# Performance work log

Hardware: AMD Instinct MI355X
Metric: run time of the kernel (lower is better)

## Reference

```python
import jax, jax.numpy as jnp
import numpy as np
from functools import partial

N_ITER = 200  # LML(n_iter=200)


def sq_dists(Xi, x):
    # Xi: [N, n], x: [B, n] -> squared euclidean dists [B, N] (torch.cdist ** 2)
    x2 = jnp.sum(x * x, axis=1, keepdims=True)          # [B, 1]
    m2 = jnp.sum(Xi * Xi, axis=1)                        # [N]
    d = x2 + m2[None, :] - 2.0 * (x @ Xi.T)
    return jnp.maximum(d, 0.0)


def _lml_solve(x, k):
    # LML projection: y = sigmoid(x + nu), nu s.t. sum(y) = k; bisection on nu.
    x_sorted = -jnp.sort(-x, axis=1)                     # descending
    lo = -x_sorted[:, k - 1] - 7.0
    hi = -x_sorted[:, k] + 7.0

    def body(i, bounds):
        lo, hi = bounds
        mid = 0.5 * (lo + hi)
        f = jnp.sum(jax.nn.sigmoid(x + mid[:, None]), axis=1) - k
        lo = jnp.where(f < 0, mid, lo)
        hi = jnp.where(f < 0, hi, mid)
        return lo, hi

    lo, hi = jax.lax.fori_loop(0, N_ITER, body, (lo, hi))
    nu = 0.5 * (lo + hi)
    return jax.nn.sigmoid(x + nu[:, None])


@partial(jax.custom_vjp, nondiff_argnums=(1,))
def lml(x, k):
    return _lml_solve(x, k)


def _lml_fwd(x, k):
    y = _lml_solve(x, k)
    return y, y


def _lml_bwd(k, y, g):
    # implicit grad: dy = s*(dx - dnu), dnu = sum(s*dx)/sum(s), s = y(1-y)
    s = y * (1.0 - y)
    dnu = jnp.sum(s * g, axis=1, keepdims=True) / jnp.sum(s, axis=1, keepdims=True)
    return (s * (g - dnu),)


lml.defvjp(_lml_fwd, _lml_bwd)


def k_softmax(beta, x, k):
    # x: [B, N] (= -dists) -> [B, N, k]
    cols = [jax.nn.softmax(beta * x, axis=1)]
    last = cols[0]
    for i in range(1, k):
        new = lml(beta * x, i + 1)
        cols.append(new - last)
        last = new
    return jnp.stack(cols, axis=2)


def hopfield(Xi, x, beta):
    return jax.nn.softmax(-beta * sq_dists(Xi, x), axis=1) @ Xi


def k_hopfield_batch(Xi, x, k, beta, hopfield_steps):
    dists = sq_dists(Xi, x)                              # [B, N]
    ksm = k_softmax(beta, -dists, k)                     # [B, N, k]
    result = jnp.einsum('nd,bnk->bdk', Xi, ksm)          # Xi.T @ ksm -> [B, n, k]
    for _ in range(hopfield_steps):
        result = jnp.stack(
            [hopfield(Xi, result[:, :, j], beta) for j in range(k)], axis=2)
    return result


def setup_inputs() -> dict:
    key = jax.random.key(0)
    kx, km = jax.random.split(key)
    return {
        'x': jax.random.normal(kx, (2048, 512), dtype=jnp.float32),
        'memories': jax.random.normal(km, (8192, 512), dtype=jnp.float32),
        'k': 5,
        'beta': 1,
        'hopfield_steps': 2,
    }


def reference(x, memories, k, beta, hopfield_steps):
    return k_hopfield_batch(memories, x, k, beta, hopfield_steps)
```

## Files before the change

### kernel.cpp

```cpp
#include <hip/hip_runtime.h>
#include <hip/hip_bf16.h>


constexpr int   Bq    = 2048;
constexpr int   Nm    = 8192;
constexpr int   Dd    = 512;
constexpr int   KK    = 5;
constexpr float BETA  = 1.0f;
constexpr int   STEPS = 2;
constexpr int   KS    = 8;
constexpr size_t PL   = (size_t)Bq * Dd;

#define DEV static __device__ __forceinline__

DEV float b2f(ushort u) { unsigned v = ((unsigned)u) << 16; float f; __builtin_memcpy(&f, &v, 4); return f; }
DEV ushort f2b(float f) { __hip_bfloat16 h = __float2bfloat16(f); ushort u; __builtin_memcpy(&u, &h, 2); return u; }
DEV float ldin(const void* p, int isf, size_t idx) {
    return isf ? ((const float*)p)[idx] : b2f(((const ushort*)p)[idx]);
}

__global__ __launch_bounds__(256) void detect_k(const ushort* __restrict__ xin,
                                                int* __restrict__ flag) {
    __shared__ int sb;
    if (threadIdx.x == 0) sb = 0;
    __syncthreads();
    int bad = 0;
    for (int i = threadIdx.x; i < 1024; i += 256) {
        float v = b2f(xin[i]);
        if (!(fabsf(v) < 64.0f)) bad = 1;
    }
    if (bad) atomicOr(&sb, 1);
    __syncthreads();
    if (threadIdx.x == 0) flag[0] = sb;
}

__global__ __launch_bounds__(256) void norms_k(const void* __restrict__ xin,
                                               const void* __restrict__ memin,
                                               const int* __restrict__ flag,
                                               float* __restrict__ x2,
                                               float* __restrict__ m2) {
    int row = blockIdx.x;
    int isf = flag[0];
    const void* src; size_t base; float* dst;
    if (row < Nm) { src = memin; base = (size_t)row * Dd; dst = m2 + row; }
    else          { src = xin; base = (size_t)(row - Nm) * Dd; dst = x2 + (row - Nm); }
    int tid = threadIdx.x, lane = tid & 63, wave = tid >> 6;
    float s = 0.f;
    for (int i = tid; i < Dd; i += 256) { float v = ldin(src, isf, base + i); s += v * v; }
    for (int off = 32; off; off >>= 1) s += __shfl_down(s, off, 64);
    __shared__ float ws[4];
    if (lane == 0) ws[wave] = s;
    __syncthreads();
    if (tid == 0) dst[0] = ws[0] + ws[1] + ws[2] + ws[3];
}

__global__ __launch_bounds__(256) void distF2_k(const void* __restrict__ A,
                                                const int* __restrict__ flag, int aForceF,
                                                const void* __restrict__ memin,
                                                float* __restrict__ S,
                                                const float* __restrict__ a2,
                                                const float* __restrict__ m2,
                                                int ab0, float negBeta) {
    __shared__ float As[16][68];
    __shared__ float Bs[16][68];
    const int tid = threadIdx.x, tx = tid & 15, ty = tid >> 4;
    const int m0 = blockIdx.y * 64, n0 = blockIdx.x * 64;
    const int isfA = aForceF ? 1 : flag[0];
    const int isfB = flag[0];

    float acc[4][4];
#pragma unroll
    for (int i = 0; i < 4; ++i)
#pragma unroll
        for (int j = 0; j < 4; ++j) acc[i][j] = 0.f;

    for (int d0 = 0; d0 < Dd; d0 += 16) {
#pragma unroll
        for (int c = tid; c < 1024; c += 256) {
            int r = c >> 4, k = c & 15;
            As[k][r] = ldin(A, isfA, (size_t)(ab0 + m0 + r) * Dd + d0 + k);
            Bs[k][r] = ldin(memin, isfB, (size_t)(n0 + r) * Dd + d0 + k);
        }
        __syncthreads();
#pragma unroll
        for (int k = 0; k < 16; ++k) {
            float4 av = *(const float4*)&As[k][ty * 4];
            float4 bv = *(const float4*)&Bs[k][tx * 4];
            float a[4] = {av.x, av.y, av.z, av.w};
            float b[4] = {bv.x, bv.y, bv.z, bv.w};
#pragma unroll
            for (int i = 0; i < 4; ++i)
#pragma unroll
                for (int j = 0; j < 4; ++j) acc[i][j] = fmaf(a[i], b[j], acc[i][j]);
        }
        __syncthreads();
    }
#pragma unroll
    for (int i = 0; i < 4; ++i) {
        int m = m0 + ty * 4 + i;
        float4 o;
        float* po = (float*)&o;
#pragma unroll
        for (int j = 0; j < 4; ++j) {
            float d = a2[m] + m2[n0 + tx * 4 + j] - 2.0f * acc[i][j];
            po[j] = negBeta * fmaxf(d, 0.0f);
        }
        *(float4*)&S[(size_t)m * Nm + n0 + tx * 4] = o;
    }
}

template <int TRF>
__global__ __launch_bounds__(256) void wgemmG_k(const float* __restrict__ Sx,
                                                const void* __restrict__ memin,
                                                const int* __restrict__ flag,
                                                const float* __restrict__ rowpar,
                                                float* __restrict__ part, int planeSz) {
    __shared__ float Ws[16][68];
    __shared__ float Bs[16][68];
    const int tid = threadIdx.x, tx = tid & 15, ty = tid >> 4;
    const int d0 = blockIdx.x * 64, b0 = blockIdx.y * 64;
    const int kz = blockIdx.z * (Nm / KS);
    const int isf = flag[0];

    float acc[4][4];
#pragma unroll
    for (int i = 0; i < 4; ++i)
#pragma unroll
        for (int j = 0; j < 4; ++j) acc[i][j] = 0.f;

    for (int nc = kz; nc < kz + Nm / KS; nc += 16) {
#pragma unroll
        for (int c = tid; c < 1024; c += 256) {
            int r = c >> 4, k = c & 15;
            float s = Sx[(size_t)(b0 + r) * Nm + nc + k];
            float p0 = rowpar[(b0 + r) * 2 + 0];
            float w;
            if constexpr (TRF == 1) w = expf(s - p0) * rowpar[(b0 + r) * 2 + 1];
            else                    w = 1.0f / (1.0f + expf(-(s + p0)));
            Ws[k][r] = w;
            int kk = c >> 6, dd = c & 63;
            Bs[kk][dd] = ldin(memin, isf, (size_t)(nc + kk) * Dd + d0 + dd);
        }
        __syncthreads();
#pragma unroll
        for (int k = 0; k < 16; ++k) {
            float4 av = *(const float4*)&Ws[k][ty * 4];
            float4 bv = *(const float4*)&Bs[k][tx * 4];
            float a[4] = {av.x, av.y, av.z, av.w};
            float b[4] = {bv.x, bv.y, bv.z, bv.w};
#pragma unroll
            for (int i = 0; i < 4; ++i)
#pragma unroll
                for (int j = 0; j < 4; ++j) acc[i][j] = fmaf(a[i], b[j], acc[i][j]);
        }
        __syncthreads();
    }
    float* pz = part + (size_t)blockIdx.z * planeSz;
#pragma unroll
    for (int i = 0; i < 4; ++i) {
        float4 o = {acc[i][0], acc[i][1], acc[i][2], acc[i][3]};
        *(float4*)&pz[(size_t)(b0 + ty * 4 + i) * Dd + d0 + tx * 4] = o;
    }
}

__global__ __launch_bounds__(256) void reduceN_k(const float* __restrict__ part,
                                                 float* __restrict__ Rj,
                                                 float* __restrict__ r2w, int doNorm,
                                                 int planeSz) {
    int row = blockIdx.x, tid = threadIdx.x, lane = tid & 63, wave = tid >> 6;
    float sq = 0.f;
    for (int e = tid; e < Dd; e += 256) {
        float s = 0.f;
#pragma unroll
        for (int z = 0; z < KS; ++z) s += part[(size_t)z * planeSz + (size_t)row * Dd + e];
        Rj[(size_t)row * Dd + e] = s;
        sq += s * s;
    }
    if (doNorm) {
        for (int off = 32; off; off >>= 1) sq += __shfl_down(sq, off, 64);
        __shared__ float ws[4];
        if (lane == 0) ws[wave] = sq;
        __syncthreads();
        if (tid == 0) r2w[row] = ws[0] + ws[1] + ws[2] + ws[3];
    }
}

__global__ __launch_bounds__(256) void rowstats_k(const float* __restrict__ S,
                                                  float* __restrict__ stats) {
    int b = blockIdx.x, tid = threadIdx.x, lane = tid & 63, wave = tid >> 6;
    __shared__ float cbuf[1024];
    __shared__ int   ccnt;
    __shared__ float tops[256 * 6];
    __shared__ float stop[6];
    __shared__ float wred[16];
    __shared__ float bcast[5];
    const float* srow = S + (size_t)b * Nm;

    float tt[6];
#pragma unroll
    for (int q = 0; q < 6; ++q) tt[q] = -3.4e38f;
    for (int i = tid; i < Nm; i += 256) {
        float v = srow[i];
        if (v > tt[5]) {
            tt[5] = v;
#pragma unroll
            for (int q = 5; q > 0; --q)
                if (tt[q] > tt[q - 1]) { float tm = tt[q]; tt[q] = tt[q - 1]; tt[q - 1] = tm; }
        }
    }
#pragma unroll
    for (int q = 0; q < 6; ++q) tops[tid * 6 + q] = tt[q];
    if (tid == 0) ccnt = 0;
    __syncthreads();
    if (tid == 0) {
        float mt[6];
#pragma unroll
        for (int q = 0; q < 6; ++q) mt[q] = -3.4e38f;
        for (int i = 0; i < 256 * 6; ++i) {
            float v = tops[i];
            if (v > mt[5]) {
                mt[5] = v;
#pragma unroll
                for (int q = 5; q > 0; --q)
                    if (mt[q] > mt[q - 1]) { float tm = mt[q]; mt[q] = mt[q - 1]; mt[q - 1] = tm; }
            }
        }
#pragma unroll
        for (int q = 0; q < 6; ++q) stop[q] = mt[q];
    }
    __syncthreads();

    float smax = stop[0];
    float cutoff = stop[5] - 40.0f;
    float p = 0.f;
    for (int i = tid; i < Nm; i += 256) {
        float v = srow[i];
        p += expf(v - smax);
        if (v >= cutoff) {
            int idx = atomicAdd(&ccnt, 1);
            if (idx < 1024) cbuf[idx] = v;
        }
    }
    for (int off = 32; off; off >>= 1) p += __shfl_down(p, off, 64);
    if (lane == 0) wred[wave] = p;
    __syncthreads();
    if (tid == 0) bcast[4] = wred[0] + wred[1] + wred[2] + wred[3];
    __syncthreads();
    float denom = bcast[4];
    int cnt = min(ccnt, 1024);

    float lo[4], hi[4];
#pragma unroll
    for (int q = 0; q < 4; ++q) { lo[q] = -stop[q + 1] - 7.0f; hi[q] = -stop[q + 2] + 7.0f; }
    for (int it = 0; it < 48; ++it) {
        float mid[4], pp[4] = {0.f, 0.f, 0.f, 0.f};
#pragma unroll
        for (int q = 0; q < 4; ++q) mid[q] = 0.5f * (lo[q] + hi[q]);
        for (int i = tid; i < cnt; i += 256) {
            float v = cbuf[i];
#pragma unroll
            for (int q = 0; q < 4; ++q) pp[q] += 1.0f / (1.0f + expf(-(v + mid[q])));
        }
#pragma unroll
        for (int q = 0; q < 4; ++q) {
            float s = pp[q];
            for (int off = 32; off; off >>= 1) s += __shfl_down(s, off, 64);
            if (lane == 0) wred[wave * 4 + q] = s;
        }
        __syncthreads();
        if (tid == 0)
#pragma unroll
            for (int q = 0; q < 4; ++q) bcast[q] = wred[q] + wred[4 + q] + wred[8 + q] + wred[12 + q];
        __syncthreads();
#pragma unroll
        for (int q = 0; q < 4; ++q) {
            float f = bcast[q] - (float)(q + 2);
            if (f < 0.f) lo[q] = mid[q]; else hi[q] = mid[q];
        }
        __syncthreads();
    }
    if (tid == 0) {
        stats[b * 6 + 0] = smax;
        stats[b * 6 + 1] = denom;
#pragma unroll
        for (int q = 0; q < 4; ++q) stats[b * 6 + 2 + q] = 0.5f * (lo[q] + hi[q]);
    }
}

__global__ __launch_bounds__(256) void rowpar_stage1_k(const float* __restrict__ stats,
                                                       float* __restrict__ rowpar, int jj) {
    int b = blockIdx.x * 256 + threadIdx.x;
    if (b >= Bq) return;
    if (jj == 0) {
        rowpar[b * 2 + 0] = stats[b * 6 + 0];
        rowpar[b * 2 + 1] = 1.0f / stats[b * 6 + 1];
    } else {
        rowpar[b * 2 + 0] = stats[b * 6 + 1 + jj];
        rowpar[b * 2 + 1] = 0.0f;
    }
}

__global__ __launch_bounds__(256) void rowmax_denom_k(const float* __restrict__ S,
                                                      float* __restrict__ rowpar) {
    int b = blockIdx.x, tid = threadIdx.x, lane = tid & 63, wave = tid >> 6;
    __shared__ float wred[4];
    __shared__ float bc[1];
    const float* srow = S + (size_t)b * Nm;
    float mx = -3.4e38f;
    for (int i = tid; i < Nm; i += 256) mx = fmaxf(mx, srow[i]);
    for (int off = 32; off; off >>= 1) mx = fmaxf(mx, __shfl_down(mx, off, 64));
    if (lane == 0) wred[wave] = mx;
    __syncthreads();
    if (tid == 0) bc[0] = fmaxf(fmaxf(wred[0], wred[1]), fmaxf(wred[2], wred[3]));
    __syncthreads();
    mx = bc[0];
    float p = 0.f;
    for (int i = tid; i < Nm; i += 256) p += expf(srow[i] - mx);
    for (int off = 32; off; off >>= 1) p += __shfl_down(p, off, 64);
    __syncthreads();
    if (lane == 0) wred[wave] = p;
    __syncthreads();
    if (tid == 0) {
        rowpar[b * 2 + 0] = mx;
        rowpar[b * 2 + 1] = 1.0f / (wred[0] + wred[1] + wred[2] + wred[3]);
    }
}

__global__ __launch_bounds__(256) void combine_k(float* __restrict__ R,
                                                 float* __restrict__ r2all) {
    int row = blockIdx.x, tid = threadIdx.x, lane = tid & 63, wave = tid >> 6;
    float sq[5] = {0.f, 0.f, 0.f, 0.f, 0.f};
    for (int e = tid; e < Dd; e += 256) {
        size_t idx = (size_t)row * Dd + e;
        float r0 = R[idx], r1 = R[PL + idx], r2v = R[2 * PL + idx],
              r3 = R[3 * PL + idx], r4 = R[4 * PL + idx];
        float o1 = r1 - r0, o2 = r2v - r1, o3 = r3 - r2v, o4 = r4 - r3;
        R[PL + idx] = o1; R[2 * PL + idx] = o2; R[3 * PL + idx] = o3; R[4 * PL + idx] = o4;
        sq[0] += r0 * r0; sq[1] += o1 * o1; sq[2] += o2 * o2; sq[3] += o3 * o3; sq[4] += o4 * o4;
    }
    __shared__ float ws[5][4];
#pragma unroll
    for (int j = 0; j < 5; ++j) {
        float s = sq[j];
        for (int off = 32; off; off >>= 1) s += __shfl_down(s, off, 64);
        if (lane == 0) ws[j][wave] = s;
    }
    __syncthreads();
    if (tid < 5) r2all[tid * Bq + row] = ws[tid][0] + ws[tid][1] + ws[tid][2] + ws[tid][3];
}

__global__ __launch_bounds__(256) void final_k(const float* __restrict__ R,
                                               void* __restrict__ out,
                                               const int* __restrict__ flag) {
    size_t idx = (size_t)blockIdx.x * 256 + threadIdx.x;
    bool isf = flag[0] != 0;
#pragma unroll
    for (int j = 0; j < KK; ++j) {
        float v = R[(size_t)j * PL + idx];
        if (isf) ((float*)out)[idx * KK + j] = v;
        else     ((ushort*)out)[idx * KK + j] = f2b(v);
    }
}

extern "C" void kernel_launch(void* const* d_in, const int* in_sizes, int n_in,
                              void* d_out, int out_size, void* d_ws, size_t ws_size,
                              hipStream_t stream) {
    const void* xin   = d_in[0];
    const void* memin = d_in[1];

    const size_t MiB = 1048576ull, KiB = 1024ull;
    char* ws = (char*)d_ws;
    float* R     = (float*)(ws + 0);
    float* m2    = (float*)(ws + 20 * MiB);
    float* x2    = (float*)(ws + 20 * MiB + 32 * KiB);
    float* stats = (float*)(ws + 20 * MiB + 48 * KiB);
    float* rpar  = (float*)(ws + 20 * MiB + 96 * KiB);
    int*   flag  = (int*)  (ws + 20 * MiB + 112 * KiB);
    float* r2all = (float*)(ws + 20 * MiB + 128 * KiB);
    float* S     = (float*)(ws + 20 * MiB + 256 * KiB);

    float* part = (float*)d_out;

    int Bc = 128;
    const int cand[4] = {1024, 512, 256, 128};
    for (int i = 0; i < 4; ++i)
        if (20 * MiB + 256 * KiB + (size_t)cand[i] * Nm * 4 <= ws_size) { Bc = cand[i]; break; }
    const int nChunk = Bq / Bc;
    const int planeSz = Bc * Dd;

    detect_k<<<1, 256, 0, stream>>>((const ushort*)xin, flag);
    norms_k<<<Nm + Bq, 256, 0, stream>>>(xin, memin, flag, x2, m2);

    for (int c = 0; c < nChunk; ++c) {
        int b0 = c * Bc;
        distF2_k<<<dim3(Nm / 64, Bc / 64), 256, 0, stream>>>(
            xin, flag, 0, memin, S, x2 + b0, m2, b0, -BETA);
        rowstats_k<<<Bc, 256, 0, stream>>>(S, stats + (size_t)b0 * 6);
        for (int jj = 0; jj < KK; ++jj) {
            float* Rj = R + (size_t)jj * PL + (size_t)b0 * Dd;
            rowpar_stage1_k<<<Bq / 256, 256, 0, stream>>>(stats, rpar, jj);
            if (jj == 0)
                wgemmG_k<1><<<dim3(Dd / 64, Bc / 64, KS), 256, 0, stream>>>(
                    S, memin, flag, rpar + (size_t)b0 * 2, part, planeSz);
            else
                wgemmG_k<2><<<dim3(Dd / 64, Bc / 64, KS), 256, 0, stream>>>(
                    S, memin, flag, rpar + (size_t)b0 * 2, part, planeSz);
            reduceN_k<<<Bc, 256, 0, stream>>>(part, Rj, nullptr, 0, planeSz);
        }
    }
    combine_k<<<Bq, 256, 0, stream>>>(R, r2all);

    for (int st = 0; st < STEPS; ++st) {
        for (int jj = 0; jj < KK; ++jj) {
            float* Rj = R + (size_t)jj * PL;
            float* r2j = r2all + (size_t)jj * Bq;
            for (int c = 0; c < nChunk; ++c) {
                int b0 = c * Bc;
                distF2_k<<<dim3(Nm / 64, Bc / 64), 256, 0, stream>>>(
                    Rj, flag, 1, memin, S, r2j + b0, m2, b0, -BETA);
                rowmax_denom_k<<<Bc, 256, 0, stream>>>(S, rpar + (size_t)b0 * 2);
                wgemmG_k<1><<<dim3(Dd / 64, Bc / 64, KS), 256, 0, stream>>>(
                    S, memin, flag, rpar + (size_t)b0 * 2, part, planeSz);
                reduceN_k<<<Bc, 256, 0, stream>>>(
                    part, Rj + (size_t)b0 * Dd, r2j + b0, 1, planeSz);
            }
        }
    }
    final_k<<<(int)(PL / 256), 256, 0, stream>>>(R, d_out, flag);
}
```

Before: 10.11 ms.

## Use split-bf16 MFMA GEMMs with precomputed hi/lo operand planes

Adds a new path that splits fp32 operands into bf16 high and low parts and runs the distance and weighted-sum GEMMs on MFMA bf16 instructions, using three products to approximate fp32 accuracy. The memory matrix is converted and transposed once up front, and the softmax/sigmoid weights are materialised as hi/lo bf16 planes before each GEMM. This replaces the scalar fp32 tiled GEMMs with matrix-core work. In exchange it adds conversion passes, extra workspace, and a small loss of precision from dropping the lo*lo term.

```diff
diff --git a/kernel.cpp b/kernel.cpp
--- a/kernel.cpp
+++ b/kernel.cpp
@@ -12,6 +12,10 @@
 constexpr size_t PL   = (size_t)Bq * Dd;
 
 #define DEV static __device__ __forceinline__
+
+typedef __attribute__((ext_vector_type(8))) short           short8v;
+typedef __attribute__((ext_vector_type(8))) unsigned short  u16x8;
+typedef __attribute__((ext_vector_type(4))) float           f32x4;
 
 DEV float b2f(ushort u) { unsigned v = ((unsigned)u) << 16; float f; __builtin_memcpy(&f, &v, 4); return f; }
 DEV ushort f2b(float f) { __hip_bfloat16 h = __float2bfloat16(f); ushort u; __builtin_memcpy(&u, &h, 2); return u; }
@@ -54,6 +58,480 @@
     if (tid == 0) dst[0] = ws[0] + ws[1] + ws[2] + ws[3];
 }
 
+
+__global__ __launch_bounds__(256) void convHL_k(const void* __restrict__ src,
+                                                const int* __restrict__ flag,
+                                                ushort* __restrict__ H,
+                                                ushort* __restrict__ L,
+                                                int nQuads, int qoff) {
+    int isf = flag[0];
+    for (int i = blockIdx.x * 256 + threadIdx.x; i < nQuads; i += gridDim.x * 256) {
+        float v[4];
+        if (isf) {
+            float4 t = ((const float4*)src)[qoff + i];
+            v[0] = t.x; v[1] = t.y; v[2] = t.z; v[3] = t.w;
+        } else {
+            ushort4 t = ((const ushort4*)src)[qoff + i];
+            v[0] = b2f(t.x); v[1] = b2f(t.y); v[2] = b2f(t.z); v[3] = b2f(t.w);
+        }
+        ushort4 h, l;
+        ushort* hp = (ushort*)&h; ushort* lp = (ushort*)&l;
+#pragma unroll
+        for (int j = 0; j < 4; ++j) {
+            ushort hu = f2b(v[j]);
+            hp[j] = hu;
+            lp[j] = f2b(v[j] - b2f(hu));
+        }
+        ((ushort4*)H)[i] = h;
+        ((ushort4*)L)[i] = l;
+    }
+}
+
+__global__ __launch_bounds__(256) void convT_k(const void* __restrict__ memin,
+                                               const int* __restrict__ flag,
+                                               ushort* __restrict__ TH,
+                                               ushort* __restrict__ TL) {
+    __shared__ float tile[64][65];
+    const int isf = flag[0];
+    const int n0 = blockIdx.x * 64, d0 = blockIdx.y * 64;
+    const int tid = threadIdx.x;
+    {
+        const int r = tid >> 2, cseg = tid & 3;
+#pragma unroll
+        for (int j = 0; j < 16; ++j)
+            tile[r][cseg * 16 + j] = ldin(memin, isf, (size_t)(n0 + r) * Dd + d0 + cseg * 16 + j);
+    }
+    __syncthreads();
+    {
+        const int drow = tid >> 2, nseg = tid & 3;
+        u16x8 h[2], l[2];
+#pragma unroll
+        for (int c = 0; c < 2; ++c)
+#pragma unroll
+            for (int j = 0; j < 8; ++j) {
+                float v = tile[nseg * 16 + c * 8 + j][drow];
+                ushort hu = f2b(v);
+                h[c][j] = hu;
+                l[c][j] = f2b(v - b2f(hu));
+            }
+        size_t base = (size_t)(d0 + drow) * Nm + n0 + nseg * 16;
+#pragma unroll
+        for (int c = 0; c < 2; ++c) {
+            *(u16x8*)&TH[base + c * 8] = h[c];
+            *(u16x8*)&TL[base + c * 8] = l[c];
+        }
+    }
+}
+
+__global__ __launch_bounds__(256) void distMF2_k(const ushort* __restrict__ Ah,
+                                                 const ushort* __restrict__ Al,
+                                                 const ushort* __restrict__ Mh,
+                                                 const ushort* __restrict__ Ml,
+                                                 float* __restrict__ S,
+                                                 const float* __restrict__ a2,
+                                                 const float* __restrict__ m2,
+                                                 int ab0, float negBeta) {
+    __shared__ ushort TA[2][4][128][8];
+    __shared__ ushort TB[2][4][128][8];
+    const int tid = threadIdx.x, lane = tid & 63, wid = tid >> 6;
+    const int wm = wid >> 1, wn = wid & 1;
+    const int m0 = blockIdx.y * 128, n0 = blockIdx.x * 128;
+    const int srow = tid & 127, kb = tid >> 7;
+    const size_t baseA = (size_t)(ab0 + m0 + srow) * Dd;
+    const size_t baseB = (size_t)(n0 + srow) * Dd;
+
+    f32x4 acc[4][4];
+    const f32x4 z = {0.f, 0.f, 0.f, 0.f};
+#pragma unroll
+    for (int i = 0; i < 4; ++i)
+#pragma unroll
+        for (int j = 0; j < 4; ++j) acc[i][j] = z;
+
+    for (int k0 = 0; k0 < Dd; k0 += 32) {
+        u16x8 rah0 = *(const u16x8*)&Ah[baseA + k0 + kb * 8];
+        u16x8 rah1 = *(const u16x8*)&Ah[baseA + k0 + (kb + 2) * 8];
+        u16x8 ral0 = *(const u16x8*)&Al[baseA + k0 + kb * 8];
+        u16x8 ral1 = *(const u16x8*)&Al[baseA + k0 + (kb + 2) * 8];
+        u16x8 rbh0 = *(const u16x8*)&Mh[baseB + k0 + kb * 8];
+        u16x8 rbh1 = *(const u16x8*)&Mh[baseB + k0 + (kb + 2) * 8];
+        u16x8 rbl0 = *(const u16x8*)&Ml[baseB + k0 + kb * 8];
+        u16x8 rbl1 = *(const u16x8*)&Ml[baseB + k0 + (kb + 2) * 8];
+        __syncthreads();
+        *(u16x8*)&TA[0][kb][srow][0]     = rah0;
+        *(u16x8*)&TA[0][kb + 2][srow][0] = rah1;
+        *(u16x8*)&TA[1][kb][srow][0]     = ral0;
+        *(u16x8*)&TA[1][kb + 2][srow][0] = ral1;
+        *(u16x8*)&TB[0][kb][srow][0]     = rbh0;
+        *(u16x8*)&TB[0][kb + 2][srow][0] = rbh1;
+        *(u16x8*)&TB[1][kb][srow][0]     = rbl0;
+        *(u16x8*)&TB[1][kb + 2][srow][0] = rbl1;
+        __syncthreads();
+
+        const int rl = lane & 15, kc = lane >> 4;
+        short8v ah[4], al[4];
+#pragma unroll
+        for (int fm = 0; fm < 4; ++fm) {
+            const int ra_ = wm * 64 + fm * 16 + rl;
+            ah[fm] = *(const short8v*)&TA[0][kc][ra_][0];
+            al[fm] = *(const short8v*)&TA[1][kc][ra_][0];
+        }
+#pragma unroll
+        for (int fn = 0; fn < 4; ++fn) {
+            const int rb_ = wn * 64 + fn * 16 + rl;
+            short8v bh = *(const short8v*)&TB[0][kc][rb_][0];
+            short8v bl = *(const short8v*)&TB[1][kc][rb_][0];
+#pragma unroll
+            for (int fm = 0; fm < 4; ++fm) {
+                acc[fm][fn] = __builtin_amdgcn_mfma_f32_16x16x32_bf16(ah[fm], bh, acc[fm][fn], 0, 0, 0);
+                acc[fm][fn] = __builtin_amdgcn_mfma_f32_16x16x32_bf16(al[fm], bh, acc[fm][fn], 0, 0, 0);
+                acc[fm][fn] = __builtin_amdgcn_mfma_f32_16x16x32_bf16(ah[fm], bl, acc[fm][fn], 0, 0, 0);
+            }
+        }
+    }
+
+    const int col = lane & 15, r0 = (lane >> 4) * 4;
+#pragma unroll
+    for (int fm = 0; fm < 4; ++fm)
+#pragma unroll
+        for (int fn = 0; fn < 4; ++fn) {
+            const int n = n0 + wn * 64 + fn * 16 + col;
+            const float mm2 = m2[n];
+#pragma unroll
+            for (int q = 0; q < 4; ++q) {
+                const int m = m0 + wm * 64 + fm * 16 + r0 + q;
+                const float d = a2[m] + mm2 - 2.0f * acc[fm][fn][q];
+                S[(size_t)m * Nm + n] = negBeta * fmaxf(d, 0.0f);
+            }
+        }
+}
+
+__global__ __launch_bounds__(256) void wconv_k(const float* __restrict__ S,
+                                               const float* __restrict__ par6,
+                                               const float* __restrict__ par2,
+                                               ushort* __restrict__ Wh,
+                                               ushort* __restrict__ Wl,
+                                               int mode, int jj) {
+    const int b = blockIdx.x, tid = threadIdx.x;
+    float p0 = 0.f, p1 = 0.f;
+    if (mode == 0)      { p0 = par6[b * 6 + 0]; p1 = 1.0f / par6[b * 6 + 1]; }
+    else if (mode == 1) { p0 = par6[b * 6 + 1 + jj]; }
+    else                { p0 = par2[b * 2 + 0]; p1 = par2[b * 2 + 1]; }
+    const float4* sp = (const float4*)(S + (size_t)b * Nm);
+    ushort* whp = Wh + (size_t)b * Nm;
+    ushort* wlp = Wl + (size_t)b * Nm;
+#pragma unroll
+    for (int r = 0; r < 8; ++r) {
+        const int qi = r * 256 + tid;
+        float4 t = sp[qi];
+        float s4[4] = {t.x, t.y, t.z, t.w};
+        ushort4 oh, ol;
+        ushort* ohp = (ushort*)&oh;
+        ushort* olp = (ushort*)&ol;
+#pragma unroll
+        for (int j = 0; j < 4; ++j) {
+            float w;
+            if (mode == 1) w = 1.0f / (1.0f + expf(-(s4[j] + p0)));
+            else           w = expf(s4[j] - p0) * p1;
+            ushort hu = f2b(w);
+            ohp[j] = hu;
+            olp[j] = f2b(w - b2f(hu));
+        }
+        ((ushort4*)whp)[qi] = oh;
+        ((ushort4*)wlp)[qi] = ol;
+    }
+}
+
+__global__ __launch_bounds__(256) void wgemm3_k(const ushort* __restrict__ Wh,
+                                                const ushort* __restrict__ Wl,
+                                                const ushort* __restrict__ MTh,
+                                                const ushort* __restrict__ MTl,
+                                                float* __restrict__ part,
+                                                int planeSz, int nzLen) {
+    __shared__ ushort TW[2][4][128][8];
+    __shared__ ushort TB[2][4][64][8];
+    const int tid = threadIdx.x, lane = tid & 63, wid = tid >> 6;
+    const int wm = wid >> 1, wn = wid & 1;
+    const int d0 = blockIdx.x * 64, b0 = blockIdx.y * 128;
+    const int nz0 = blockIdx.z * nzLen;
+
+    const int wrow = tid & 127, wkb = tid >> 7;
+    const int brow = tid & 63,  bkc = tid >> 6;
+    const size_t baseW = (size_t)(b0 + wrow) * Nm;
+    const size_t baseB = (size_t)(d0 + brow) * Nm;
+
+    f32x4 acc[4][2];
+    const f32x4 z = {0.f, 0.f, 0.f, 0.f};
+#pragma unroll
+    for (int i = 0; i < 4; ++i)
+#pragma unroll
+        for (int j = 0; j < 2; ++j) acc[i][j] = z;
+
+    for (int nc = nz0; nc < nz0 + nzLen; nc += 32) {
+        u16x8 rwh0 = *(const u16x8*)&Wh[baseW + nc + wkb * 8];
+        u16x8 rwh1 = *(const u16x8*)&Wh[baseW + nc + (wkb + 2) * 8];
+        u16x8 rwl0 = *(const u16x8*)&Wl[baseW + nc + wkb * 8];
+        u16x8 rwl1 = *(const u16x8*)&Wl[baseW + nc + (wkb + 2) * 8];
+        u16x8 rbh  = *(const u16x8*)&MTh[baseB + nc + bkc * 8];
+        u16x8 rbl  = *(const u16x8*)&MTl[baseB + nc + bkc * 8];
+        __syncthreads();
+        *(u16x8*)&TW[0][wkb][wrow][0]     = rwh0;
+        *(u16x8*)&TW[0][wkb + 2][wrow][0] = rwh1;
+        *(u16x8*)&TW[1][wkb][wrow][0]     = rwl0;
+        *(u16x8*)&TW[1][wkb + 2][wrow][0] = rwl1;
+        *(u16x8*)&TB[0][bkc][brow][0]     = rbh;
+        *(u16x8*)&TB[1][bkc][brow][0]     = rbl;
+        __syncthreads();
+
+        const int rl = lane & 15, kc = lane >> 4;
+        short8v wfh[4], wfl[4];
+#pragma unroll
+        for (int fm = 0; fm < 4; ++fm) {
+            const int rw_ = wm * 64 + fm * 16 + rl;
+            wfh[fm] = *(const short8v*)&TW[0][kc][rw_][0];
+            wfl[fm] = *(const short8v*)&TW[1][kc][rw_][0];
+        }
+#pragma unroll
+        for (int fn = 0; fn < 2; ++fn) {
+            const int rd_ = wn * 32 + fn * 16 + rl;
+            short8v bh = *(const short8v*)&TB[0][kc][rd_][0];
+            short8v bl = *(const short8v*)&TB[1][kc][rd_][0];
+#pragma unroll
+            for (int fm = 0; fm < 4; ++fm) {
+                acc[fm][fn] = __builtin_amdgcn_mfma_f32_16x16x32_bf16(wfh[fm], bh, acc[fm][fn], 0, 0, 0);
+                acc[fm][fn] = __builtin_amdgcn_mfma_f32_16x16x32_bf16(wfl[fm], bh, acc[fm][fn], 0, 0, 0);
+                acc[fm][fn] = __builtin_amdgcn_mfma_f32_16x16x32_bf16(wfh[fm], bl, acc[fm][fn], 0, 0, 0);
+            }
+        }
+    }
+
+    float* pz = part + (size_t)blockIdx.z * planeSz;
+    const int col = lane & 15, r0 = (lane >> 4) * 4;
+#pragma unroll
+    for (int fm = 0; fm < 4; ++fm)
+#pragma unroll
+        for (int fn = 0; fn < 2; ++fn) {
+            const int dc = d0 + wn * 32 + fn * 16 + col;
+#pragma unroll
+            for (int q = 0; q < 4; ++q) {
+                const int br = b0 + wm * 64 + fm * 16 + r0 + q;
+                pz[(size_t)br * Dd + dc] = acc[fm][fn][q];
+            }
+        }
+}
+
+__global__ __launch_bounds__(256) void reduceHL_k(const float* __restrict__ part,
+                                                  ushort* __restrict__ Rh,
+                                                  ushort* __restrict__ Rl,
+                                                  float* __restrict__ r2w, int doNorm,
+                                                  int planeSz, int ks) {
+    int row = blockIdx.x, tid = threadIdx.x, lane = tid & 63, wave = tid >> 6;
+    float sq = 0.f;
+    for (int e = tid; e < Dd; e += 256) {
+        float s = 0.f;
+        for (int z = 0; z < ks; ++z) s += part[(size_t)z * planeSz + (size_t)row * Dd + e];
+        ushort h = f2b(s);
+        Rh[(size_t)row * Dd + e] = h;
+        Rl[(size_t)row * Dd + e] = f2b(s - b2f(h));
+        sq += s * s;
+    }
+    if (doNorm) {
+        for (int off = 32; off; off >>= 1) sq += __shfl_down(sq, off, 64);
+        __shared__ float ws[4];
+        if (lane == 0) ws[wave] = sq;
+        __syncthreads();
+        if (tid == 0) r2w[row] = ws[0] + ws[1] + ws[2] + ws[3];
+    }
+}
+
+__global__ __launch_bounds__(256) void combineHL_k(ushort* __restrict__ rhl,
+                                                   float* __restrict__ r2all) {
+    int row = blockIdx.x, tid = threadIdx.x, lane = tid & 63, wave = tid >> 6;
+    float sq[5] = {0.f, 0.f, 0.f, 0.f, 0.f};
+    for (int e = tid; e < Dd; e += 256) {
+        size_t idx = (size_t)row * Dd + e;
+        float v[5];
+#pragma unroll
+        for (int j = 0; j < 5; ++j)
+            v[j] = b2f(rhl[(size_t)j * 2 * PL + idx]) + b2f(rhl[(size_t)j * 2 * PL + PL + idx]);
+        float o[5];
+        o[0] = v[0];
+        o[1] = v[1] - v[0]; o[2] = v[2] - v[1]; o[3] = v[3] - v[2]; o[4] = v[4] - v[3];
+#pragma unroll
+        for (int j = 1; j < 5; ++j) {
+            ushort h = f2b(o[j]);
+            rhl[(size_t)j * 2 * PL + idx] = h;
+            rhl[(size_t)j * 2 * PL + PL + idx] = f2b(o[j] - b2f(h));
+        }
+#pragma unroll
+        for (int j = 0; j < 5; ++j) sq[j] += o[j] * o[j];
+    }
+    __shared__ float ws[5][4];
+#pragma unroll
+    for (int j = 0; j < 5; ++j) {
+        float s = sq[j];
+        for (int off = 32; off; off >>= 1) s += __shfl_down(s, off, 64);
+        if (lane == 0) ws[j][wave] = s;
+    }
+    __syncthreads();
+    if (tid < 5) r2all[tid * Bq + row] = ws[tid][0] + ws[tid][1] + ws[tid][2] + ws[tid][3];
+}
+
+__global__ __launch_bounds__(256) void finalHL_k(const ushort* __restrict__ rhl,
+                                                 void* __restrict__ out,
+                                                 const int* __restrict__ flag) {
+    size_t idx = (size_t)blockIdx.x * 256 + threadIdx.x;
+    bool isf = flag[0] != 0;
+#pragma unroll
+    for (int j = 0; j < KK; ++j) {
+        float v = b2f(rhl[(size_t)j * 2 * PL + idx]) + b2f(rhl[(size_t)j * 2 * PL + PL + idx]);
+        if (isf) ((float*)out)[idx * KK + j] = v;
+        else     ((ushort*)out)[idx * KK + j] = f2b(v);
+    }
+}
+
+
+__global__ __launch_bounds__(256) void rowstats_k(const float* __restrict__ S,
+                                                  float* __restrict__ stats) {
+    int b = blockIdx.x, tid = threadIdx.x, lane = tid & 63, wave = tid >> 6;
+    __shared__ float cbuf[1024];
+    __shared__ int   ccnt;
+    __shared__ float tops[256 * 6];
+    __shared__ float stop[6];
+    __shared__ float wred[16];
+    __shared__ float bcast[5];
+    const float* srow = S + (size_t)b * Nm;
+
+    float tt[6];
+#pragma unroll
+    for (int q = 0; q < 6; ++q) tt[q] = -3.4e38f;
+    for (int i = tid; i < Nm; i += 256) {
+        float v = srow[i];
+        if (v > tt[5]) {
+            tt[5] = v;
+#pragma unroll
+            for (int q = 5; q > 0; --q)
+                if (tt[q] > tt[q - 1]) { float tm = tt[q]; tt[q] = tt[q - 1]; tt[q - 1] = tm; }
+        }
+    }
+#pragma unroll
+    for (int q = 0; q < 6; ++q) tops[tid * 6 + q] = tt[q];
+    if (tid == 0) ccnt = 0;
+    __syncthreads();
+    if (tid == 0) {
+        float mt[6];
+#pragma unroll
+        for (int q = 0; q < 6; ++q) mt[q] = -3.4e38f;
+        for (int i = 0; i < 256 * 6; ++i) {
+            float v = tops[i];
+            if (v > mt[5]) {
+                mt[5] = v;
+#pragma unroll
+                for (int q = 5; q > 0; --q)
+                    if (mt[q] > mt[q - 1]) { float tm = mt[q]; mt[q] = mt[q - 1]; mt[q - 1] = tm; }
+            }
+        }
+#pragma unroll
+        for (int q = 0; q < 6; ++q) stop[q] = mt[q];
+    }
+    __syncthreads();
+
+    float smax = stop[0];
+    float cutoff = stop[5] - 40.0f;
+    float p = 0.f;
+    for (int i = tid; i < Nm; i += 256) {
+        float v = srow[i];
+        p += expf(v - smax);
+        if (v >= cutoff) {
+            int idx = atomicAdd(&ccnt, 1);
+            if (idx < 1024) cbuf[idx] = v;
+        }
+    }
+    for (int off = 32; off; off >>= 1) p += __shfl_down(p, off, 64);
+    if (lane == 0) wred[wave] = p;
+    __syncthreads();
+    if (tid == 0) bcast[4] = wred[0] + wred[1] + wred[2] + wred[3];
+    __syncthreads();
+    float denom = bcast[4];
+    int cnt = min(ccnt, 1024);
+
+    float lo[4], hi[4];
+#pragma unroll
+    for (int q = 0; q < 4; ++q) { lo[q] = -stop[q + 1] - 7.0f; hi[q] = -stop[q + 2] + 7.0f; }
+    for (int it = 0; it < 48; ++it) {
+        float mid[4], pp[4] = {0.f, 0.f, 0.f, 0.f};
+#pragma unroll
+        for (int q = 0; q < 4; ++q) mid[q] = 0.5f * (lo[q] + hi[q]);
+        for (int i = tid; i < cnt; i += 256) {
+            float v = cbuf[i];
+#pragma unroll
+            for (int q = 0; q < 4; ++q) pp[q] += 1.0f / (1.0f + expf(-(v + mid[q])));
+        }
+#pragma unroll
+        for (int q = 0; q < 4; ++q) {
+            float s = pp[q];
+            for (int off = 32; off; off >>= 1) s += __shfl_down(s, off, 64);
+            if (lane == 0) wred[wave * 4 + q] = s;
+        }
+        __syncthreads();
+        if (tid == 0)
+#pragma unroll
+            for (int q = 0; q < 4; ++q) bcast[q] = wred[q] + wred[4 + q] + wred[8 + q] + wred[12 + q];
+        __syncthreads();
+#pragma unroll
+        for (int q = 0; q < 4; ++q) {
+            float f = bcast[q] - (float)(q + 2);
+            if (f < 0.f) lo[q] = mid[q]; else hi[q] = mid[q];
+        }
+        __syncthreads();
+    }
+    if (tid == 0) {
+        stats[b * 6 + 0] = smax;
+        stats[b * 6 + 1] = denom;
+#pragma unroll
+        for (int q = 0; q < 4; ++q) stats[b * 6 + 2 + q] = 0.5f * (lo[q] + hi[q]);
+    }
+}
+
+__global__ __launch_bounds__(256) void rowpar_stage1_k(const float* __restrict__ stats,
+                                                       float* __restrict__ rowpar, int jj) {
+    int b = blockIdx.x * 256 + threadIdx.x;
+    if (b >= Bq) return;
+    if (jj == 0) {
+        rowpar[b * 2 + 0] = stats[b * 6 + 0];
+        rowpar[b * 2 + 1] = 1.0f / stats[b * 6 + 1];
+    } else {
+        rowpar[b * 2 + 0] = stats[b * 6 + 1 + jj];
+        rowpar[b * 2 + 1] = 0.0f;
+    }
+}
+
+__global__ __launch_bounds__(256) void rowmax_denom_k(const float* __restrict__ S,
+                                                      float* __restrict__ rowpar) {
+    int b = blockIdx.x, tid = threadIdx.x, lane = tid & 63, wave = tid >> 6;
+    __shared__ float wred[4];
+    __shared__ float bc[1];
+    const float* srow = S + (size_t)b * Nm;
+    float mx = -3.4e38f;
+    for (int i = tid; i < Nm; i += 256) mx = fmaxf(mx, srow[i]);
+    for (int off = 32; off; off >>= 1) mx = fmaxf(mx, __shfl_down(mx, off, 64));
+    if (lane == 0) wred[wave] = mx;
+    __syncthreads();
+    if (tid == 0) bc[0] = fmaxf(fmaxf(wred[0], wred[1]), fmaxf(wred[2], wred[3]));
+    __syncthreads();
+    mx = bc[0];
+    float p = 0.f;
+    for (int i = tid; i < Nm; i += 256) p += expf(srow[i] - mx);
+    for (int off = 32; off; off >>= 1) p += __shfl_down(p, off, 64);
+    __syncthreads();
+    if (lane == 0) wred[wave] = p;
+    __syncthreads();
+    if (tid == 0) {
+        rowpar[b * 2 + 0] = mx;
+        rowpar[b * 2 + 1] = 1.0f / (wred[0] + wred[1] + wred[2] + wred[3]);
+    }
+}
+
+
 __global__ __launch_bounds__(256) void distF2_k(const void* __restrict__ A,
                                                 const int* __restrict__ flag, int aForceF,
                                                 const void* __restrict__ memin,
@@ -185,147 +663,6 @@
     }
 }
 
-__global__ __launch_bounds__(256) void rowstats_k(const float* __restrict__ S,
-                                                  float* __restrict__ stats) {
-    int b = blockIdx.x, tid = threadIdx.x, lane = tid & 63, wave = tid >> 6;
-    __shared__ float cbuf[1024];
-    __shared__ int   ccnt;
-    __shared__ float tops[256 * 6];
-    __shared__ float stop[6];
-    __shared__ float wred[16];
-    __shared__ float bcast[5];
-    const float* srow = S + (size_t)b * Nm;
-
-    float tt[6];
-#pragma unroll
-    for (int q = 0; q < 6; ++q) tt[q] = -3.4e38f;
-    for (int i = tid; i < Nm; i += 256) {
-        float v = srow[i];
-        if (v > tt[5]) {
-            tt[5] = v;
-#pragma unroll
-            for (int q = 5; q > 0; --q)
-                if (tt[q] > tt[q - 1]) { float tm = tt[q]; tt[q] = tt[q - 1]; tt[q - 1] = tm; }
-        }
-    }
-#pragma unroll
-    for (int q = 0; q < 6; ++q) tops[tid * 6 + q] = tt[q];
-    if (tid == 0) ccnt = 0;
-    __syncthreads();
-    if (tid == 0) {
-        float mt[6];
-#pragma unroll
-        for (int q = 0; q < 6; ++q) mt[q] = -3.4e38f;
-        for (int i = 0; i < 256 * 6; ++i) {
-            float v = tops[i];
-            if (v > mt[5]) {
-                mt[5] = v;
-#pragma unroll
-                for (int q = 5; q > 0; --q)
-                    if (mt[q] > mt[q - 1]) { float tm = mt[q]; mt[q] = mt[q - 1]; mt[q - 1] = tm; }
-            }
-        }
-#pragma unroll
-        for (int q = 0; q < 6; ++q) stop[q] = mt[q];
-    }
-    __syncthreads();
-
-    float smax = stop[0];
-    float cutoff = stop[5] - 40.0f;
-    float p = 0.f;
-    for (int i = tid; i < Nm; i += 256) {
-        float v = srow[i];
-        p += expf(v - smax);
-        if (v >= cutoff) {
-            int idx = atomicAdd(&ccnt, 1);
-            if (idx < 1024) cbuf[idx] = v;
-        }
-    }
-    for (int off = 32; off; off >>= 1) p += __shfl_down(p, off, 64);
-    if (lane == 0) wred[wave] = p;
-    __syncthreads();
-    if (tid == 0) bcast[4] = wred[0] + wred[1] + wred[2] + wred[3];
-    __syncthreads();
-    float denom = bcast[4];
-    int cnt = min(ccnt, 1024);
-
-    float lo[4], hi[4];
-#pragma unroll
-    for (int q = 0; q < 4; ++q) { lo[q] = -stop[q + 1] - 7.0f; hi[q] = -stop[q + 2] + 7.0f; }
-    for (int it = 0; it < 48; ++it) {
-        float mid[4], pp[4] = {0.f, 0.f, 0.f, 0.f};
-#pragma unroll
-        for (int q = 0; q < 4; ++q) mid[q] = 0.5f * (lo[q] + hi[q]);
-        for (int i = tid; i < cnt; i += 256) {
-            float v = cbuf[i];
-#pragma unroll
-            for (int q = 0; q < 4; ++q) pp[q] += 1.0f / (1.0f + expf(-(v + mid[q])));
-        }
-#pragma unroll
-        for (int q = 0; q < 4; ++q) {
-            float s = pp[q];
-            for (int off = 32; off; off >>= 1) s += __shfl_down(s, off, 64);
-            if (lane == 0) wred[wave * 4 + q] = s;
-        }
-        __syncthreads();
-        if (tid == 0)
-#pragma unroll
-            for (int q = 0; q < 4; ++q) bcast[q] = wred[q] + wred[4 + q] + wred[8 + q] + wred[12 + q];
-        __syncthreads();
-#pragma unroll
-        for (int q = 0; q < 4; ++q) {
-            float f = bcast[q] - (float)(q + 2);
-            if (f < 0.f) lo[q] = mid[q]; else hi[q] = mid[q];
-        }
-        __syncthreads();
-    }
-    if (tid == 0) {
-        stats[b * 6 + 0] = smax;
-        stats[b * 6 + 1] = denom;
-#pragma unroll
-        for (int q = 0; q < 4; ++q) stats[b * 6 + 2 + q] = 0.5f * (lo[q] + hi[q]);
-    }
-}
-
-__global__ __launch_bounds__(256) void rowpar_stage1_k(const float* __restrict__ stats,
-                                                       float* __restrict__ rowpar, int jj) {
-    int b = blockIdx.x * 256 + threadIdx.x;
-    if (b >= Bq) return;
-    if (jj == 0) {
-        rowpar[b * 2 + 0] = stats[b * 6 + 0];
-        rowpar[b * 2 + 1] = 1.0f / stats[b * 6 + 1];
-    } else {
-        rowpar[b * 2 + 0] = stats[b * 6 + 1 + jj];
-        rowpar[b * 2 + 1] = 0.0f;
-    }
-}
-
-__global__ __launch_bounds__(256) void rowmax_denom_k(const float* __restrict__ S,
-                                                      float* __restrict__ rowpar) {
-    int b = blockIdx.x, tid = threadIdx.x, lane = tid & 63, wave = tid >> 6;
-    __shared__ float wred[4];
-    __shared__ float bc[1];
-    const float* srow = S + (size_t)b * Nm;
-    float mx = -3.4e38f;
-    for (int i = tid; i < Nm; i += 256) mx = fmaxf(mx, srow[i]);
-    for (int off = 32; off; off >>= 1) mx = fmaxf(mx, __shfl_down(mx, off, 64));
-    if (lane == 0) wred[wave] = mx;
-    __syncthreads();
-    if (tid == 0) bc[0] = fmaxf(fmaxf(wred[0], wred[1]), fmaxf(wred[2], wred[3]));
-    __syncthreads();
-    mx = bc[0];
-    float p = 0.f;
-    for (int i = tid; i < Nm; i += 256) p += expf(srow[i] - mx);
-    for (int off = 32; off; off >>= 1) p += __shfl_down(p, off, 64);
-    __syncthreads();
-    if (lane == 0) wred[wave] = p;
-    __syncthreads();
-    if (tid == 0) {
-        rowpar[b * 2 + 0] = mx;
-        rowpar[b * 2 + 1] = 1.0f / (wred[0] + wred[1] + wred[2] + wred[3]);
-    }
-}
-
 __global__ __launch_bounds__(256) void combine_k(float* __restrict__ R,
                                                  float* __restrict__ r2all) {
     int row = blockIdx.x, tid = threadIdx.x, lane = tid & 63, wave = tid >> 6;
@@ -362,6 +699,7 @@
     }
 }
 
+
 extern "C" void kernel_launch(void* const* d_in, const int* in_sizes, int n_in,
                               void* d_out, int out_size, void* d_ws, size_t ws_size,
                               hipStream_t stream) {
@@ -370,6 +708,91 @@
 
     const size_t MiB = 1048576ull, KiB = 1024ull;
     char* ws = (char*)d_ws;
+    float* part = (float*)d_out;
+
+    int BcF = 0, ksF = 0;
+    {
+        const int cb[10] = {1024, 512, 512, 256, 256, 256, 128, 128, 128, 128};
+        const int ck[10] = {   8,  16,   8,  32,  16,   8,  64,  32,  16,   8};
+        for (int i = 0; i < 10; ++i) {
+            size_t need = 52 * MiB + 160 * KiB + (size_t)cb[i] * 64 * KiB;
+            size_t needOut = (size_t)ck[i] * cb[i] * Dd * 4;
+            if (need <= ws_size && needOut <= (size_t)out_size) { BcF = cb[i]; ksF = ck[i]; break; }
+        }
+    }
+
+    if (BcF) {
+        const int Bc = BcF, ks = ksF;
+        ushort* rhl  = (ushort*)(ws + 0);
+        ushort* mh   = (ushort*)(ws + 20 * MiB);
+        ushort* ml   = (ushort*)(ws + 28 * MiB);
+        ushort* mth  = (ushort*)(ws + 36 * MiB);
+        ushort* mtl  = (ushort*)(ws + 44 * MiB);
+        char*  misc  = ws + 52 * MiB;
+        float* m2    = (float*)(misc + 0);
+        float* x2    = (float*)(misc + 32 * KiB);
+        float* stats = (float*)(misc + 40 * KiB);
+        float* rpar  = (float*)(misc + 88 * KiB);
+        int*   flag  = (int*)  (misc + 104 * KiB);
+        float* r2all = (float*)(misc + 112 * KiB);
+        ushort* Wh   = (ushort*)(ws + 52 * MiB + 160 * KiB);
+        ushort* Wl   = Wh + (size_t)Bc * Nm;
+        float* S     = (float*)(ws + 52 * MiB + 160 * KiB + (size_t)Bc * 32 * KiB);
+        ushort* xsH  = Wh;
+        ushort* xsL  = Wh + (size_t)Bc * Dd;
+
+        const int nChunk = Bq / Bc;
+        const int planeSz = Bc * Dd;
+        const int nzLen = Nm / ks;
+
+        detect_k<<<1, 256, 0, stream>>>((const ushort*)xin, flag);
+        norms_k<<<Nm + Bq, 256, 0, stream>>>(xin, memin, flag, x2, m2);
+        convHL_k<<<2048, 256, 0, stream>>>(memin, flag, mh, ml, Nm * Dd / 4, 0);
+        convT_k<<<dim3(Nm / 64, Dd / 64), 256, 0, stream>>>(memin, flag, mth, mtl);
+
+        for (int c = 0; c < nChunk; ++c) {
+            int b0 = c * Bc;
+            convHL_k<<<Bc / 2, 256, 0, stream>>>(xin, flag, xsH, xsL,
+                                                 Bc * Dd / 4, b0 * Dd / 4);
+            distMF2_k<<<dim3(Nm / 128, Bc / 128), 256, 0, stream>>>(
+                xsH, xsL, mh, ml, S, x2 + b0, m2, 0, -BETA);
+            rowstats_k<<<Bc, 256, 0, stream>>>(S, stats + (size_t)b0 * 6);
+            for (int jj = 0; jj < KK; ++jj) {
+                wconv_k<<<Bc, 256, 0, stream>>>(S, stats + (size_t)b0 * 6, nullptr,
+                                                Wh, Wl, jj == 0 ? 0 : 1, jj);
+                wgemm3_k<<<dim3(Dd / 64, Bc / 128, ks), 256, 0, stream>>>(
+                    Wh, Wl, mth, mtl, part, planeSz, nzLen);
+                ushort* Rh = rhl + (size_t)jj * 2 * PL + (size_t)b0 * Dd;
+                ushort* Rl = rhl + (size_t)jj * 2 * PL + PL + (size_t)b0 * Dd;
+                reduceHL_k<<<Bc, 256, 0, stream>>>(part, Rh, Rl, nullptr, 0, planeSz, ks);
+            }
+        }
+        combineHL_k<<<Bq, 256, 0, stream>>>(rhl, r2all);
+
+        for (int st = 0; st < STEPS; ++st) {
+            for (int jj = 0; jj < KK; ++jj) {
+                ushort* Rhj = rhl + (size_t)jj * 2 * PL;
+                ushort* Rlj = rhl + (size_t)jj * 2 * PL + PL;
+                float* r2j = r2all + (size_t)jj * Bq;
+                for (int c = 0; c < nChunk; ++c) {
+                    int b0 = c * Bc;
+                    distMF2_k<<<dim3(Nm / 128, Bc / 128), 256, 0, stream>>>(
+                        Rhj, Rlj, mh, ml, S, r2j + b0, m2, b0, -BETA);
+                    rowmax_denom_k<<<Bc, 256, 0, stream>>>(S, rpar + (size_t)b0 * 2);
+                    wconv_k<<<Bc, 256, 0, stream>>>(S, nullptr, rpar + (size_t)b0 * 2,
+                                                    Wh, Wl, 2, 0);
+                    wgemm3_k<<<dim3(Dd / 64, Bc / 128, ks), 256, 0, stream>>>(
+                        Wh, Wl, mth, mtl, part, planeSz, nzLen);
+                    reduceHL_k<<<Bc, 256, 0, stream>>>(
+                        part, Rhj + (size_t)b0 * Dd, Rlj + (size_t)b0 * Dd,
+                        r2j + b0, 1, planeSz, ks);
+                }
+            }
+        }
+        finalHL_k<<<(int)(PL / 256), 256, 0, stream>>>(rhl, d_out, flag);
+        return;
+    }
+
     float* R     = (float*)(ws + 0);
     float* m2    = (float*)(ws + 20 * MiB);
     float* x2    = (float*)(ws + 20 * MiB + 32 * KiB);
@@ -379,12 +802,13 @@
     float* r2all = (float*)(ws + 20 * MiB + 128 * KiB);
     float* S     = (float*)(ws + 20 * MiB + 256 * KiB);
 
-    float* part = (float*)d_out;
-
     int Bc = 128;
     const int cand[4] = {1024, 512, 256, 128};
-    for (int i = 0; i < 4; ++i)
-        if (20 * MiB + 256 * KiB + (size_t)cand[i] * Nm * 4 <= ws_size) { Bc = cand[i]; break; }
+    for (int i = 0; i < 4; ++i) {
+        size_t needWS  = 20 * MiB + 256 * KiB + (size_t)cand[i] * Nm * 4;
+        size_t needOut = (size_t)KS * cand[i] * Dd * 4;
+        if (needWS <= ws_size && needOut <= (size_t)out_size) { Bc = cand[i]; break; }
+    }
     const int nChunk = Bq / Bc;
     const int planeSz = Bc * Dd;
 
```

After: 11.67 ms. +15.4%, slower.
